# Optimization experiments

Measured on AMD Instinct MI355X. Metric: run time of the kernel, lower is better.

Reference implementation:

```python
import jax, jax.numpy as jnp
import numpy as np
from math import comb

F = 32           # features
NB = 8           # num_basis_functions
N_ITER = 3       # num_iterations
CUTOFF = 5.0
MAXZ = 17        # max_atomic_number
NDCM = 4
N_NODES = 10000
N_EDGES = 160000
OFF = (0, 1, 4)  # start index of degree l block in the (L+1)^2=9 axis
WID = (1, 3, 5)
DEG = np.array([0, 1, 1, 1, 2, 2, 2, 2, 2])


def _sph_harm(u):
    # Real spherical harmonics up to l=2, Racah normalization, cartesian order.
    x, y, z = u[..., 0], u[..., 1], u[..., 2]
    s3 = 3.0 ** 0.5
    return jnp.stack([
        jnp.ones_like(x),
        x, y, z,
        s3 * x * y, s3 * y * z, 0.5 * (3.0 * z * z - 1.0), s3 * x * z,
        0.5 * s3 * (x * x - y * y),
    ], axis=-1)


def _gaunt():
    # Exact Gaunt (triple-product) coupling coefficients via spherical quadrature:
    # Gauss-Legendre (8 pts) in cos(theta) x 16 uniform pts in phi is exact for
    # products of three degree<=2 harmonics. Odd-parity (l1+l2+l3 odd) entries
    # integrate to zero, which matches include_pseudotensors=False.
    t, w = np.polynomial.legendre.leggauss(8)
    phi = np.arange(16) * (2.0 * np.pi / 16.0)
    st = np.sqrt(1.0 - t * t)
    pts = np.stack([
        st[:, None] * np.cos(phi)[None, :],
        st[:, None] * np.sin(phi)[None, :],
        t[:, None] * np.ones_like(phi)[None, :],
    ], axis=-1).reshape(-1, 3)
    wts = np.repeat(w / 32.0, 16)  # mean over sphere
    Y = np.asarray(_sph_harm(jnp.asarray(pts)))
    G = np.einsum('k,kp,kq,kr->pqr', wts, Y, Y, Y)
    G[np.abs(G) < 1e-10] = 0.0
    return G.astype(np.float32)


GAUNT = _gaunt()  # (9, 9, 9)
MP_PATHS = [(a, b, c) for a in range(3) for b in range(3) for c in range(3)
            if (a + b + c) % 2 == 0 and abs(a - b) <= c <= a + b]
TD_PATHS = [p for p in MP_PATHS if p[2] <= 1]


def _blk(l):
    return slice(OFF[l], OFF[l] + WID[l])


def _edge_basis(positions, dst_idx, src_idx):
    d = positions[src_idx] - positions[dst_idx]          # (E, 3)
    r2 = jnp.sum(d * d, axis=-1)
    r = jnp.sqrt(jnp.maximum(r2, 1e-12))
    Y = _sph_harm(d / r[:, None])                        # (E, 9)
    rc = jnp.minimum(r, CUTOFF - 1e-6)                   # safe smooth_cutoff
    cut = jnp.where(r < CUTOFF,
                    jnp.exp(-(rc * rc) / ((CUTOFF - rc) * (CUTOFF + rc))), 0.0)
    yv = 1.0 / (1.0 + r)                                 # reciprocal mapping
    k = jnp.arange(NB)
    binom = jnp.asarray([float(comb(NB - 1, i)) for i in range(NB)], dtype=jnp.float32)
    rbf = binom * yv[:, None] ** k * (1.0 - yv[:, None]) ** (NB - 1 - k)
    return Y, rbf * cut[:, None]                         # (E,9), (E,NB)


def _message_pass(x, Y, rbf, dst_idx, src_idx, W, num_nodes):
    # msg[e,lm3,f] = sum G[lm1,lm2,lm3] x_src[e,lm1,f] Y[e,lm2] (rbf[e] @ W[l1,l2,l3])[f]
    xs = x[src_idx]                                      # (E, 9, F)
    parts = {0: [], 1: [], 2: []}
    for (l1, l2, l3) in MP_PATHS:
        rw = rbf @ W[l1, l2, l3]                         # (E, F) radial weights
        t = xs[:, _blk(l1), :] * rw[:, None, :]
        c = jnp.einsum('pqr,epf,eq->erf',
                       GAUNT[_blk(l1), _blk(l2), _blk(l3)], t, Y[:, _blk(l2)])
        parts[l3].append(c)
    msg = jnp.concatenate([sum(parts[l]) for l in range(3)], axis=1)
    return jax.ops.segment_sum(msg, dst_idx, num_segments=num_nodes)


def _dense(x, W, b):
    out = jnp.einsum('npf,pfg->npg', x, W[DEG])
    return out.at[:, 0, :].add(b)


def _silu_e3(x):
    # Gated equivariant silu: act(s) on scalars, x_lm * act'(s) for l>0.
    s = x[:, 0:1, :]
    sg = jax.nn.sigmoid(s)
    return jnp.concatenate([s * sg, x[:, 1:, :] * (sg * (1.0 + s * (1.0 - sg)))], axis=1)


def _tensor_dense(x, W):
    # with per-path feature-mixing weights; output (N, 4, NDCM).
    parts = {0: [], 1: []}
    for (l1, l2, l3) in TD_PATHS:
        c = jnp.einsum('pqr,npf,nqf,fg->nrg',
                       GAUNT[_blk(l1), _blk(l2), _blk(l3)],
                       x[:, _blk(l1), :], x[:, _blk(l2), :], W[l1, l2, l3])
        parts[l3].append(c)
    return jnp.concatenate([sum(parts[0]), sum(parts[1])], axis=1)


def _forward(positions, embed_table, mp_W, d1_W, d1_b, d2_W, d2_b, td_W,
             mono_W, element_bias, atomic_numbers, dst_idx, src_idx):
    n = positions.shape[0]
    Y, rbf = _edge_basis(positions, dst_idx, src_idx)
    x = jnp.zeros((n, 9, F), positions.dtype).at[:, 0, :].set(embed_table[atomic_numbers])
    for i in range(N_ITER):
        y = x + _message_pass(x, Y, rbf, dst_idx, src_idx, mp_W[i], n)
        y = _silu_e3(_dense(y, d1_W[i], d1_b[i]))
        y = _dense(y, d2_W[i], d2_b[i])
        x = x + y
    x2 = _tensor_dense(x, td_W)                          # (n, 4, NDCM)
    atomic_mono = x2[:, 0, :] @ mono_W + element_bias[atomic_numbers][:, None]
    # gated hard_tanh then * 0.3; dipole = l=1 components
    s = x2[:, 0:1, :]
    gate = ((s > -1.0) & (s < 1.0)).astype(x2.dtype)
    xh = jnp.concatenate([jnp.clip(s, -1.0, 1.0), x2[:, 1:, :] * gate], axis=1) * 0.3
    atomic_dipo = xh[:, 1:4, :]                          # (n, 3, NDCM)
    return atomic_mono, atomic_dipo


def setup_inputs() -> dict:
    key = jax.random.key(0)
    ks = jax.random.split(key, 12)
    atomic_numbers = jax.random.randint(ks[0], (N_NODES,), 0, MAXZ + 1)
    positions = jax.random.normal(ks[1], (N_NODES, 3), jnp.float32)
    dst_idx = jax.random.randint(ks[2], (N_EDGES,), 0, N_NODES)
    src_idx = jax.random.randint(ks[3], (N_EDGES,), 0, N_NODES)
    src_idx = jnp.where(src_idx == dst_idx, (src_idx + 1) % N_NODES, src_idx)
    embed_table = jax.random.normal(ks[4], (MAXZ + 1, F), jnp.float32)
    mp_W = jax.random.normal(ks[5], (N_ITER, 3, 3, 3, NB, F), jnp.float32) * 0.05
    d1_W = jax.random.normal(ks[6], (N_ITER, 3, F, F), jnp.float32) * (1.0 / F ** 0.5)
    d1_b = jnp.zeros((N_ITER, F), jnp.float32)
    d2_W = jax.random.normal(ks[7], (N_ITER, 3, F, F), jnp.float32) * (1.0 / F ** 0.5)
    d2_b = jnp.zeros((N_ITER, F), jnp.float32)
    td_W = jax.random.normal(ks[8], (3, 3, 2, F, NDCM), jnp.float32) * (1.0 / F)
    mono_W = jax.random.normal(ks[9], (NDCM, NDCM), jnp.float32) * (1.0 / NDCM ** 0.5)
    element_bias = jnp.zeros((MAXZ + 1,), jnp.float32)
    return {'positions': positions, 'embed_table': embed_table, 'mp_W': mp_W,
            'd1_W': d1_W, 'd1_b': d1_b, 'd2_W': d2_W, 'd2_b': d2_b,
            'td_W': td_W, 'mono_W': mono_W, 'element_bias': element_bias,
            'atomic_numbers': atomic_numbers, 'dst_idx': dst_idx, 'src_idx': src_idx}


def reference(positions, embed_table, mp_W, d1_W, d1_b, d2_W, d2_b, td_W,
              mono_W, element_bias, atomic_numbers, dst_idx, src_idx):
    return _forward(positions, embed_table, mp_W, d1_W, d1_b, d2_W, d2_b, td_W,
                    mono_W, element_bias, atomic_numbers, dst_idx, src_idx)
```

## Files before the change

### kernel.cpp

```cpp
#include <hip/hip_runtime.h>
#include <math.h>

#define NN 10000
#define NE 160000
#define EPB 8
#define MT 256
#define CEPB 16

namespace {
constexpr int kL1[11] = {0,0,0,1,1,1,1,2,2,2,2};
constexpr int kL2[11] = {0,1,2,0,1,1,2,0,1,2,2};
constexpr int kL3[11] = {0,1,2,1,0,2,1,2,1,0,2};
constexpr int kWOFF[11] = {0,5,7,10,12,14,16,20,22,24,26};
constexpr int tL1[7] = {0,0,1,1,1,2,2};
constexpr int tL2[7] = {0,1,0,1,2,1,2};
constexpr int tL3[7] = {0,1,1,0,1,1,0};
constexpr int kOFF[3] = {0,1,4};
constexpr int kWID[3] = {1,3,5};

struct TVT { unsigned char t[35], p[35]; };
constexpr TVT makeTV() {
  TVT v{};
  int ti = 0;
  for (int t = 0; t < 11; ++t)
    for (int i = 0; i < kWID[kL1[t]]; ++i) {
      v.t[ti] = (unsigned char)t;
      v.p[ti] = (unsigned char)(kOFF[kL1[t]] + i);
      ++ti;
    }
  return v;
}
constexpr TVT TV = makeTV();

struct CTb { unsigned char r[116], tv[116]; };
constexpr CTb makeCT() {
  CTb v{};
  int c = 0, ti = 0;
  for (int t = 0; t < 11; ++t)
    for (int i = 0; i < kWID[kL1[t]]; ++i) {
      for (int k = 0; k < kWID[kL3[t]]; ++k) {
        v.r[c]  = (unsigned char)(kOFF[kL3[t]] + k);
        v.tv[c] = (unsigned char)ti;
        ++c;
      }
      ++ti;
    }
  v.r[115] = 0; v.tv[115] = 0;
  return v;
}
constexpr CTb CTC = makeCT();
}

__device__ float GAUNT_d[729];
__device__ unsigned char CT_P_d[115], CT_R_d[115], CT_L2_d[115];

__device__ __forceinline__ float sphf(int c, float x, float y, float z) {
  const float s3 = 1.7320508075688772f;
  switch (c) {
    case 0: return 1.0f;
    case 1: return x;
    case 2: return y;
    case 3: return z;
    case 4: return s3 * x * y;
    case 5: return s3 * y * z;
    case 6: return 0.5f * (3.0f * z * z - 1.0f);
    case 7: return s3 * x * z;
    default: return 0.5f * s3 * (x * x - y * y);
  }
}

__global__ void gaunt_kernel() {
  __shared__ float Ysh[128][9];
  __shared__ double cph[16], sph[16];
  __shared__ double stq[8], tsh[8], wsh[8];
  const int idx = threadIdx.x;
  const double T[8] = {-0.9602898564975363, -0.7966664774136267, -0.5255324099163290, -0.1834346424956498,
                        0.1834346424956498,  0.5255324099163290,  0.7966664774136267,  0.9602898564975363};
  const double Wq[8] = {0.1012285362903763, 0.2223810344533745, 0.3137066458778873, 0.3626837833783620,
                        0.3626837833783620, 0.3137066458778873, 0.2223810344533745, 0.1012285362903763};
  if (idx < 16) {
    double phi = (double)idx * (6.283185307179586 / 16.0);
    cph[idx] = cos(phi);
    sph[idx] = sin(phi);
  }
  if (idx < 8) {
    tsh[idx] = T[idx];
    wsh[idx] = Wq[idx] / 32.0;
    stq[idx] = sqrt(1.0 - T[idx] * T[idx]);
  }
  __syncthreads();
  for (int i = idx; i < 128 * 9; i += 768) {
    int k = i / 9, c = i - k * 9;
    int it = k >> 4, ip = k & 15;
    float xf = (float)(stq[it] * cph[ip]);
    float yf = (float)(stq[it] * sph[ip]);
    float zf = (float)tsh[it];
    Ysh[k][c] = sphf(c, xf, yf, zf);
  }
  __syncthreads();
  if (idx < 729) {
    int p = idx / 81, q = (idx / 9) % 9, r = idx % 9;
    double acc = 0.0;
    for (int k = 0; k < 128; ++k)
      acc += wsh[k >> 4] * (double)Ysh[k][p] * (double)Ysh[k][q] * (double)Ysh[k][r];
    GAUNT_d[idx] = (fabs(acc) < 1e-10) ? 0.0f : (float)acc;
  }
  if (idx == 0) {
    int c = 0;
    for (int t = 0; t < 11; ++t) {
      int l1 = kL1[t], l2 = kL2[t], l3 = kL3[t];
      for (int i = 0; i < kWID[l1]; ++i)
        for (int k = 0; k < kWID[l3]; ++k) {
          CT_P_d[c]  = (unsigned char)(kOFF[l1] + i);
          CT_R_d[c]  = (unsigned char)(kOFF[l3] + k);
          CT_L2_d[c] = (unsigned char)l2;
          ++c;
        }
    }
  }
}

__global__ void hist_kernel(const int* __restrict__ dstI, int* __restrict__ cnt) {
  int e = blockIdx.x * 256 + threadIdx.x;
  if (e < NE) atomicAdd(&cnt[dstI[e]], 1);
}

__global__ void scan_kernel(int* __restrict__ wofs) {
  __shared__ int partial[1024];
  const int tid = threadIdx.x;
  const int base = tid * 10;
  int local[10];
  int s = 0;
  #pragma unroll
  for (int i = 0; i < 10; ++i) {
    int idx = base + i;
    int v = (idx < NN) ? wofs[idx] : 0;
    local[i] = s;
    s += v;
  }
  partial[tid] = s;
  __syncthreads();
  for (int off = 1; off < 1024; off <<= 1) {
    int v = (tid >= off) ? partial[tid - off] : 0;
    __syncthreads();
    partial[tid] += v;
    __syncthreads();
  }
  int pre = (tid == 0) ? 0 : partial[tid - 1];
  #pragma unroll
  for (int i = 0; i < 10; ++i) {
    int idx = base + i;
    if (idx < NN) wofs[idx] = pre + local[i];
  }
}

__global__ void edge_kernel(const float* __restrict__ pos,
                            const int* __restrict__ srcI, const int* __restrict__ dstI,
                            int* __restrict__ wofs, int* __restrict__ ssrc, int* __restrict__ sdst,
                            float* __restrict__ Yb, float* __restrict__ Rb) {
  int e = blockIdx.x * 256 + threadIdx.x;
  if (e >= NE) return;
  int s = srcI[e], d = dstI[e];
  float dx = pos[s * 3 + 0] - pos[d * 3 + 0];
  float dy = pos[s * 3 + 1] - pos[d * 3 + 1];
  float dz = pos[s * 3 + 2] - pos[d * 3 + 2];
  float r2 = dx * dx + dy * dy + dz * dz;
  float r = sqrtf(fmaxf(r2, 1e-12f));
  float inv = 1.0f / r;
  float x = dx * inv, y = dy * inv, z = dz * inv;
  const float s3 = 1.7320508075688772f;
  int sp = atomicAdd(&wofs[d], 1);
  ssrc[sp] = s;
  sdst[sp] = d;
  Yb[sp * 9 + 0] = 1.0f;
  Yb[sp * 9 + 1] = x;
  Yb[sp * 9 + 2] = y;
  Yb[sp * 9 + 3] = z;
  Yb[sp * 9 + 4] = s3 * x * y;
  Yb[sp * 9 + 5] = s3 * y * z;
  Yb[sp * 9 + 6] = 0.5f * (3.0f * z * z - 1.0f);
  Yb[sp * 9 + 7] = s3 * x * z;
  Yb[sp * 9 + 8] = 0.5f * s3 * (x * x - y * y);
  float rc = fminf(r, 5.0f - 1e-6f);
  float cut = (r < 5.0f) ? expf(-(rc * rc) / ((5.0f - rc) * (5.0f + rc))) : 0.0f;
  float yv = 1.0f / (1.0f + r);
  float om = 1.0f - yv;
  const float binom[8] = {1.f, 7.f, 21.f, 35.f, 35.f, 21.f, 7.f, 1.f};
  float yk[8], ok[8];
  yk[0] = 1.0f; ok[0] = 1.0f;
  #pragma unroll
  for (int k = 1; k < 8; ++k) { yk[k] = yk[k - 1] * yv; ok[k] = ok[k - 1] * om; }
  #pragma unroll
  for (int k = 0; k < 8; ++k) Rb[sp * 8 + k] = binom[k] * yk[k] * ok[7 - k] * cut;
}

__global__ void coef_kernel(const float* __restrict__ Yb, float* __restrict__ Cb) {
  __shared__ float Gs[729];
  __shared__ float Ys[CEPB][9];
  __shared__ unsigned char Tp[115], Tr[115], Tl2[115];
  const int tid = threadIdx.x;
  const int e0 = blockIdx.x * CEPB;
  for (int i = tid; i < 729; i += 256) Gs[i] = GAUNT_d[i];
  for (int i = tid; i < 115; i += 256) { Tp[i] = CT_P_d[i]; Tr[i] = CT_R_d[i]; Tl2[i] = CT_L2_d[i]; }
  for (int i = tid; i < CEPB * 9; i += 256) Ys[i / 9][i % 9] = Yb[e0 * 9 + i];
  __syncthreads();
  for (int i = tid; i < CEPB * 128; i += 256) {
    int ce = i >> 7, c = i & 127;
    if (c < 116) {
      float a = 0.0f;
      if (c < 115) {
        int p = Tp[c], r = Tr[c], l2 = Tl2[c];
        int q0 = (l2 == 0) ? 0 : ((l2 == 1) ? 1 : 4);
        int nq = (l2 == 0) ? 1 : ((l2 == 1) ? 3 : 5);
        for (int j = 0; j < nq; ++j) a += Gs[(p * 9 + q0 + j) * 9 + r] * Ys[ce][q0 + j];
      }
      Cb[(size_t)(e0 + ce) * 116 + c] = a;
    }
  }
}

__global__ void init_kernel(const float* __restrict__ embed, const int* __restrict__ Z,
                            float* __restrict__ xb, float* __restrict__ yb) {
  int idx = blockIdx.x * 256 + threadIdx.x;
  if (idx >= NN * 288) return;
  int n = idx / 288;
  int rem = idx - n * 288;
  int p = rem >> 5, f = rem & 31;
  xb[idx] = (p == 0) ? embed[Z[n] * 32 + f] : 0.0f;
  yb[idx] = 0.0f;
}

__launch_bounds__(MT)
__global__ void message_kernel(const float* __restrict__ xb, float* __restrict__ yb,
                               const float* __restrict__ Rb, const float* __restrict__ Cb,
                               const float* __restrict__ Wg,
                               const int* __restrict__ ssrc, const int* __restrict__ sdst) {
  __shared__ __align__(16) float U[11 * 256];
  __shared__ __align__(16) float4 Cs4[EPB][29];
  __shared__ __align__(16) float Rs[EPB][8];
  __shared__ int Ds[EPB];
  __shared__ int Hs[EPB + 1];
  __shared__ int nseg_s;
  const int tid = threadIdx.x;
  const int e0 = blockIdx.x * EPB;
  const int le = tid >> 5, f = tid & 31;

  const int sn = ssrc[e0 + le];
  float xs[9];
  #pragma unroll
  for (int p = 0; p < 9; ++p) xs[p] = xb[sn * 288 + p * 32 + f];

  float* Ws = U;
  #pragma unroll
  for (int t = 0; t < 11; ++t) {
    const int off = kWOFF[t] * 256;
    Ws[t * 256 + tid] = Wg[off + tid];
  }
  if (tid < EPB * 29) {
    const float4* Cbv = (const float4*)Cb;
    ((float4*)Cs4)[tid] = Cbv[(size_t)e0 * 29 + tid];
  }
  for (int i = tid; i < EPB * 8; i += MT) Rs[i >> 3][i & 7] = Rb[e0 * 8 + i];
  if (tid < EPB) Ds[tid] = sdst[e0 + tid];
  __syncthreads();

  if (tid == 0) {
    int ns = 0;
    #pragma unroll
    for (int i = 0; i < EPB; ++i)
      if (i == 0 || Ds[i] != Ds[i - 1]) Hs[ns++] = i;
    Hs[ns] = EPB;
    nseg_s = ns;
  }

  const float4 R0 = *(const float4*)&Rs[le][0];
  const float4 R1 = *(const float4*)&Rs[le][4];
  float rw[11];
  #pragma unroll
  for (int t = 0; t < 11; ++t) {
    const float* base = &Ws[t * 256];
    rw[t] = R0.x * base[f] + R0.y * base[32 + f] + R0.z * base[64 + f] + R0.w * base[96 + f]
          + R1.x * base[128 + f] + R1.y * base[160 + f] + R1.z * base[192 + f] + R1.w * base[224 + f];
  }

  float tv[35];
  #pragma unroll
  for (int j = 0; j < 35; ++j) tv[j] = rw[TV.t[j]] * xs[TV.p[j]];

  float msg[9] = {0.f, 0.f, 0.f, 0.f, 0.f, 0.f, 0.f, 0.f, 0.f};
  #pragma unroll
  for (int c4 = 0; c4 < 29; ++c4) {
    const float4 cc = Cs4[le][c4];
    const int c = c4 * 4;
    msg[CTC.r[c]] += cc.x * tv[CTC.tv[c]];
    if (c + 1 < 115) msg[CTC.r[c + 1]] += cc.y * tv[CTC.tv[c + 1]];
    if (c + 2 < 115) msg[CTC.r[c + 2]] += cc.z * tv[CTC.tv[c + 2]];
    if (c + 3 < 115) msg[CTC.r[c + 3]] += cc.w * tv[CTC.tv[c + 3]];
  }

  __syncthreads();
  float* Ms = U;
  #pragma unroll
  for (int rr = 0; rr < 9; ++rr) Ms[le * 288 + rr * 32 + f] = msg[rr];
  __syncthreads();

  const int nseg = nseg_s;
  for (int i = tid; i < nseg * 288; i += MT) {
    int s = i / 288, rf = i - s * 288;
    int h = Hs[s], hend = Hs[s + 1];
    float a = 0.0f;
    for (int e = h; e < hend; ++e) a += Ms[e * 288 + rf];
    atomicAdd(&yb[Ds[h] * 288 + rf], a);
  }
}

__launch_bounds__(MT)
__global__ void message_kernel_ic(const float* __restrict__ xb, float* __restrict__ yb,
                                  const float* __restrict__ Yb, const float* __restrict__ Rb,
                                  const float* __restrict__ Wg,
                                  const int* __restrict__ ssrc, const int* __restrict__ sdst) {
  __shared__ float Gs[729];
  __shared__ float Ws[11 * 256];
  __shared__ float Ys[EPB][9];
  __shared__ float Rs[EPB][8];
  __shared__ float Cs[EPB][116];
  __shared__ float Ms[EPB][288];
  __shared__ int Ds[EPB];
  __shared__ int Hs[EPB + 1];
  __shared__ int nseg_s;
  __shared__ unsigned char Tp[115], Tr[115], Tl2[115];
  const int tid = threadIdx.x;
  const int e0 = blockIdx.x * EPB;

  for (int i = tid; i < 729; i += MT) Gs[i] = GAUNT_d[i];
  for (int i = tid; i < 115; i += MT) { Tp[i] = CT_P_d[i]; Tr[i] = CT_R_d[i]; Tl2[i] = CT_L2_d[i]; }
  #pragma unroll
  for (int t = 0; t < 11; ++t) Ws[t * 256 + tid] = Wg[kWOFF[t] * 256 + tid];
  for (int i = tid; i < EPB * 16; i += MT) {
    int le = i >> 4, q = i & 15;
    if (q < 9) Ys[le][q] = Yb[(e0 + le) * 9 + q];
  }
  for (int i = tid; i < EPB * 8; i += MT) Rs[i >> 3][i & 7] = Rb[e0 * 8 + i];
  if (tid < EPB) Ds[tid] = sdst[e0 + tid];
  __syncthreads();

  const int le = tid >> 5, f = tid & 31;
  const int sn = ssrc[e0 + le];
  float xs[9];
  #pragma unroll
  for (int p = 0; p < 9; ++p) xs[p] = xb[sn * 288 + p * 32 + f];

  for (int i = tid; i < EPB * 128; i += MT) {
    int ce = i >> 7, c = i & 127;
    if (c < 115) {
      int p = Tp[c], r = Tr[c], l2 = Tl2[c];
      int q0 = (l2 == 0) ? 0 : ((l2 == 1) ? 1 : 4);
      int nq = (l2 == 0) ? 1 : ((l2 == 1) ? 3 : 5);
      float a = 0.0f;
      for (int j = 0; j < nq; ++j) a += Gs[(p * 9 + q0 + j) * 9 + r] * Ys[ce][q0 + j];
      Cs[ce][c] = a;
    }
  }
  if (tid == 0) {
    int ns = 0;
    #pragma unroll
    for (int i = 0; i < EPB; ++i)
      if (i == 0 || Ds[i] != Ds[i - 1]) Hs[ns++] = i;
    Hs[ns] = EPB;
    nseg_s = ns;
  }
  __syncthreads();

  const float4 R0 = *(const float4*)&Rs[le][0];
  const float4 R1 = *(const float4*)&Rs[le][4];
  float rw[11];
  #pragma unroll
  for (int t = 0; t < 11; ++t) {
    const float* base = &Ws[t * 256];
    rw[t] = R0.x * base[f] + R0.y * base[32 + f] + R0.z * base[64 + f] + R0.w * base[96 + f]
          + R1.x * base[128 + f] + R1.y * base[160 + f] + R1.z * base[192 + f] + R1.w * base[224 + f];
  }
  float tv[35];
  #pragma unroll
  for (int j = 0; j < 35; ++j) tv[j] = rw[TV.t[j]] * xs[TV.p[j]];
  float msg[9] = {0.f, 0.f, 0.f, 0.f, 0.f, 0.f, 0.f, 0.f, 0.f};
  #pragma unroll
  for (int c = 0; c < 115; ++c) msg[CTC.r[c]] += Cs[le][c] * tv[CTC.tv[c]];
  #pragma unroll
  for (int rr = 0; rr < 9; ++rr) Ms[le][rr * 32 + f] = msg[rr];
  __syncthreads();

  const int nseg = nseg_s;
  for (int i = tid; i < nseg * 288; i += MT) {
    int s = i / 288, rf = i - s * 288;
    int h = Hs[s], hend = Hs[s + 1];
    float a = 0.0f;
    for (int e = h; e < hend; ++e) a += Ms[e][rf];
    atomicAdd(&yb[Ds[h] * 288 + rf], a);
  }
}

__global__ void dense_kernel(float* __restrict__ ybuf, float* __restrict__ xb,
                             const float* __restrict__ W1, const float* __restrict__ b1,
                             const float* __restrict__ W2, const float* __restrict__ b2) {
  __shared__ float yn[288];
  __shared__ float act[288];
  __shared__ float sb[32];
  const int n = blockIdx.x;
  const int tid = threadIdx.x;
  const int p = tid >> 5, g = tid & 31;
  const float xv = xb[n * 288 + tid];
  const float yv = ybuf[n * 288 + tid];
  ybuf[n * 288 + tid] = 0.0f;
  yn[tid] = xv + yv;
  __syncthreads();
  const int dg = (p == 0) ? 0 : ((p < 4) ? 1 : 2);
  float a = (p == 0) ? b1[g] : 0.0f;
  #pragma unroll
  for (int f = 0; f < 32; ++f) a += yn[p * 32 + f] * W1[(dg * 32 + f) * 32 + g];
  if (p == 0) sb[g] = a;
  __syncthreads();
  float s = sb[g];
  float sg = 1.0f / (1.0f + expf(-s));
  float v = (p == 0) ? s * sg : a * (sg * (1.0f + s * (1.0f - sg)));
  act[tid] = v;
  __syncthreads();
  float o = (p == 0) ? b2[g] : 0.0f;
  #pragma unroll
  for (int f = 0; f < 32; ++f) o += act[p * 32 + f] * W2[(dg * 32 + f) * 32 + g];
  xb[n * 288 + tid] = xv + o;
}

__global__ void final_kernel(const float* __restrict__ xb, const float* __restrict__ tdW,
                             const float* __restrict__ monoW, const float* __restrict__ ebias,
                             const int* __restrict__ Z, float* __restrict__ out) {
  __shared__ float xl[288];
  __shared__ float B[4][32];
  __shared__ float cb[16];
  const int n = blockIdx.x;
  const int tid = threadIdx.x;
  const int r = tid >> 5, f = tid & 31;
  for (int i = tid; i < 288; i += 128) xl[i] = xb[n * 288 + i];
  __syncthreads();
  float creg = 0.0f;
  #pragma unroll
  for (int t = 0; t < 7; ++t) {
    const int l1 = tL1[t], l2 = tL2[t], l3 = tL3[t];
    const bool active = (l3 == 0) ? (r == 0) : (r >= 1);
    float b = 0.0f;
    if (active) {
      #pragma unroll
      for (int i = 0; i < kWID[l1]; ++i) {
        const int p = kOFF[l1] + i;
        float xp = xl[p * 32 + f];
        #pragma unroll
        for (int j = 0; j < kWID[l2]; ++j) {
          const int q = kOFF[l2] + j;
          b += GAUNT_d[(p * 9 + q) * 9 + r] * xp * xl[q * 32 + f];
        }
      }
    }
    B[r][f] = b;
    __syncthreads();
    if (f < 4 && active) {
      const float* w = tdW + ((l1 * 3 + l2) * 2 + l3) * 128;
      float acc = 0.0f;
      #pragma unroll
      for (int f2 = 0; f2 < 32; ++f2) acc += B[r][f2] * w[f2 * 4 + f];
      creg += acc;
    }
    __syncthreads();
  }
  if (f < 4) cb[r * 4 + f] = creg;
  __syncthreads();
  if (tid < 4) {
    int g = tid;
    float m = 0.0f;
    #pragma unroll
    for (int j = 0; j < 4; ++j) m += cb[j] * monoW[j * 4 + g];
    out[n * 4 + g] = m + ebias[Z[n]];
  }
  if (tid < 12) {
    int row = tid / 4 + 1, g = tid % 4;
    float s = cb[g];
    float gate = (s > -1.0f && s < 1.0f) ? 1.0f : 0.0f;
    out[NN * 4 + n * 12 + (row - 1) * 4 + g] = cb[row * 4 + g] * gate * 0.3f;
  }
}

extern "C" void kernel_launch(void* const* d_in, const int* in_sizes, int n_in,
                              void* d_out, int out_size, void* d_ws, size_t ws_size,
                              hipStream_t stream) {
  const float* positions = (const float*)d_in[0];
  const float* embed     = (const float*)d_in[1];
  const float* mpW       = (const float*)d_in[2];
  const float* d1W       = (const float*)d_in[3];
  const float* d1b       = (const float*)d_in[4];
  const float* d2W       = (const float*)d_in[5];
  const float* d2b       = (const float*)d_in[6];
  const float* tdW       = (const float*)d_in[7];
  const float* monoW     = (const float*)d_in[8];
  const float* ebias     = (const float*)d_in[9];
  const int* Z   = (const int*)d_in[10];
  const int* dst = (const int*)d_in[11];
  const int* src = (const int*)d_in[12];
  float* out = (float*)d_out;

  float* Yb = (float*)d_ws;
  float* Rb = Yb + (size_t)NE * 9;
  float* xb = Rb + (size_t)NE * 8;
  float* yb = xb + (size_t)NN * 288;
  size_t base_f = (size_t)NE * 9 + (size_t)NE * 8 + (size_t)NN * 288 * 2;
  size_t need_pc = (base_f + (size_t)NE * 116) * 4 + ((size_t)NE * 2 + NN) * 4;
  bool pc = ws_size >= need_pc;

  float* Cb = yb + (size_t)NN * 288;
  float* after = pc ? (Cb + (size_t)NE * 116) : Cb;
  int* ssrc = (int*)after;
  int* sdst = ssrc + NE;
  int* wofs = sdst + NE;

  gaunt_kernel<<<1, 768, 0, stream>>>();
  hipMemsetAsync(wofs, 0, NN * sizeof(int), stream);
  hist_kernel<<<NE / 256, 256, 0, stream>>>(dst, wofs);
  scan_kernel<<<1, 1024, 0, stream>>>(wofs);
  edge_kernel<<<NE / 256, 256, 0, stream>>>(positions, src, dst, wofs, ssrc, sdst, Yb, Rb);
  if (pc) coef_kernel<<<NE / CEPB, 256, 0, stream>>>(Yb, Cb);
  init_kernel<<<(NN * 288 + 255) / 256, 256, 0, stream>>>(embed, Z, xb, yb);

  for (int it = 0; it < 3; ++it) {
    if (pc)
      message_kernel<<<NE / EPB, MT, 0, stream>>>(xb, yb, Rb, Cb, mpW + (size_t)it * 27 * 256, ssrc, sdst);
    else
      message_kernel_ic<<<NE / EPB, MT, 0, stream>>>(xb, yb, Yb, Rb, mpW + (size_t)it * 27 * 256, ssrc, sdst);
    dense_kernel<<<NN, 288, 0, stream>>>(yb, xb, d1W + (size_t)it * 3 * 1024, d1b + it * 32,
                                         d2W + (size_t)it * 3 * 1024, d2b + it * 32);
  }
  final_kernel<<<NN, 128, 0, stream>>>(xb, tdW, monoW, ebias, Z, out);
}
```

Before: 431.1 us.

## Process 16 edges per block with two features per thread and fuse final dense

The message kernel now handles 16 edges per 256-thread block, with each thread computing two features as packed float2 vectors. The radial-weight and coupling contraction is restructured to loop directly over path blocks instead of through precomputed tv arrays, and the segmented reduction runs in two halves that reuse the shared buffer. The last iteration's dense update is fused with the final tensor-dipole kernel, removing one launch and a round trip of node features through global memory. Fewer threads per edge and the added half-wise synchronization may reduce parallelism or raise register pressure.

```diff
diff --git a/kernel.cpp b/kernel.cpp
--- a/kernel.cpp
+++ b/kernel.cpp
@@ -3,9 +3,11 @@
 
 #define NN 10000
 #define NE 160000
-#define EPB 8
+#define MEPB 16
 #define MT 256
 #define CEPB 16
+
+typedef float float2v __attribute__((ext_vector_type(2)));
 
 namespace {
 constexpr int kL1[11] = {0,0,0,1,1,1,1,2,2,2,2};
@@ -230,25 +232,26 @@
   yb[idx] = 0.0f;
 }
 
-__launch_bounds__(MT)
+__launch_bounds__(MT, 8)
 __global__ void message_kernel(const float* __restrict__ xb, float* __restrict__ yb,
                                const float* __restrict__ Rb, const float* __restrict__ Cb,
                                const float* __restrict__ Wg,
                                const int* __restrict__ ssrc, const int* __restrict__ sdst) {
   __shared__ __align__(16) float U[11 * 256];
-  __shared__ __align__(16) float4 Cs4[EPB][29];
-  __shared__ __align__(16) float Rs[EPB][8];
-  __shared__ int Ds[EPB];
-  __shared__ int Hs[EPB + 1];
-  __shared__ int nseg_s;
+  __shared__ __align__(16) float Cs[MEPB][116];
+  __shared__ __align__(16) float Rs[MEPB][8];
+  __shared__ int Ds[MEPB];
+  __shared__ int Hs[2][9];
+  __shared__ int nsegS[2];
   const int tid = threadIdx.x;
-  const int e0 = blockIdx.x * EPB;
-  const int le = tid >> 5, f = tid & 31;
+  const int e0 = blockIdx.x * MEPB;
+  const int le = tid >> 4;
+  const int f  = (tid & 15) * 2;
 
   const int sn = ssrc[e0 + le];
-  float xs[9];
-  #pragma unroll
-  for (int p = 0; p < 9; ++p) xs[p] = xb[sn * 288 + p * 32 + f];
+  float2v xs2[9];
+  #pragma unroll
+  for (int p = 0; p < 9; ++p) xs2[p] = *(const float2v*)&xb[sn * 288 + p * 32 + f];
 
   float* Ws = U;
   #pragma unroll
@@ -256,92 +259,106 @@
     const int off = kWOFF[t] * 256;
     Ws[t * 256 + tid] = Wg[off + tid];
   }
-  if (tid < EPB * 29) {
+  {
     const float4* Cbv = (const float4*)Cb;
-    ((float4*)Cs4)[tid] = Cbv[(size_t)e0 * 29 + tid];
-  }
-  for (int i = tid; i < EPB * 8; i += MT) Rs[i >> 3][i & 7] = Rb[e0 * 8 + i];
-  if (tid < EPB) Ds[tid] = sdst[e0 + tid];
+    float4* Csv = (float4*)Cs;
+    #pragma unroll
+    for (int i = tid; i < MEPB * 29; i += MT) Csv[i] = Cbv[(size_t)e0 * 29 + i];
+  }
+  for (int i = tid; i < MEPB * 8; i += MT) Rs[i >> 3][i & 7] = Rb[e0 * 8 + i];
+  if (tid < MEPB) Ds[tid] = sdst[e0 + tid];
   __syncthreads();
 
   if (tid == 0) {
-    int ns = 0;
     #pragma unroll
-    for (int i = 0; i < EPB; ++i)
-      if (i == 0 || Ds[i] != Ds[i - 1]) Hs[ns++] = i;
-    Hs[ns] = EPB;
-    nseg_s = ns;
-  }
-
-  const float4 R0 = *(const float4*)&Rs[le][0];
-  const float4 R1 = *(const float4*)&Rs[le][4];
-  float rw[11];
+    for (int b = 0; b < 2; ++b) {
+      int ns = 0;
+      #pragma unroll
+      for (int i = 0; i < 8; ++i) {
+        int gi = b * 8 + i;
+        if (i == 0 || Ds[gi] != Ds[gi - 1]) Hs[b][ns++] = i;
+      }
+      Hs[b][ns] = 8;
+      nsegS[b] = ns;
+    }
+  }
+
+  float2v msg[9] = {{0.f,0.f},{0.f,0.f},{0.f,0.f},{0.f,0.f},{0.f,0.f},{0.f,0.f},{0.f,0.f},{0.f,0.f},{0.f,0.f}};
+  int c = 0;
   #pragma unroll
   for (int t = 0; t < 11; ++t) {
     const float* base = &Ws[t * 256];
-    rw[t] = R0.x * base[f] + R0.y * base[32 + f] + R0.z * base[64 + f] + R0.w * base[96 + f]
-          + R1.x * base[128 + f] + R1.y * base[160 + f] + R1.z * base[192 + f] + R1.w * base[224 + f];
-  }
-
-  float tv[35];
-  #pragma unroll
-  for (int j = 0; j < 35; ++j) tv[j] = rw[TV.t[j]] * xs[TV.p[j]];
-
-  float msg[9] = {0.f, 0.f, 0.f, 0.f, 0.f, 0.f, 0.f, 0.f, 0.f};
-  #pragma unroll
-  for (int c4 = 0; c4 < 29; ++c4) {
-    const float4 cc = Cs4[le][c4];
-    const int c = c4 * 4;
-    msg[CTC.r[c]] += cc.x * tv[CTC.tv[c]];
-    if (c + 1 < 115) msg[CTC.r[c + 1]] += cc.y * tv[CTC.tv[c + 1]];
-    if (c + 2 < 115) msg[CTC.r[c + 2]] += cc.z * tv[CTC.tv[c + 2]];
-    if (c + 3 < 115) msg[CTC.r[c + 3]] += cc.w * tv[CTC.tv[c + 3]];
-  }
-
-  __syncthreads();
+    float2v acc = {0.f, 0.f};
+    #pragma unroll
+    for (int k = 0; k < 8; ++k) {
+      const float rv = Rs[le][k];
+      const float2v rvv = {rv, rv};
+      const float2v w2 = *(const float2v*)&base[k * 32 + f];
+      acc = acc + rvv * w2;
+    }
+    const int o1 = kOFF[kL1[t]], w1 = kWID[kL1[t]];
+    const int o3 = kOFF[kL3[t]], w3 = kWID[kL3[t]];
+    #pragma unroll
+    for (int i = 0; i < w1; ++i) {
+      const float2v tvv = acc * xs2[o1 + i];
+      #pragma unroll
+      for (int k2 = 0; k2 < w3; ++k2) {
+        const float cc = Cs[le][c]; ++c;
+        const float2v ccv = {cc, cc};
+        msg[o3 + k2] = msg[o3 + k2] + ccv * tvv;
+      }
+    }
+  }
+
   float* Ms = U;
   #pragma unroll
-  for (int rr = 0; rr < 9; ++rr) Ms[le * 288 + rr * 32 + f] = msg[rr];
-  __syncthreads();
-
-  const int nseg = nseg_s;
-  for (int i = tid; i < nseg * 288; i += MT) {
-    int s = i / 288, rf = i - s * 288;
-    int h = Hs[s], hend = Hs[s + 1];
-    float a = 0.0f;
-    for (int e = h; e < hend; ++e) a += Ms[e * 288 + rf];
-    atomicAdd(&yb[Ds[h] * 288 + rf], a);
-  }
-}
-
-__launch_bounds__(MT)
+  for (int b = 0; b < 2; ++b) {
+    __syncthreads();
+    if ((le >> 3) == b) {
+      #pragma unroll
+      for (int rr = 0; rr < 9; ++rr)
+        *(float2v*)&Ms[(le & 7) * 288 + rr * 32 + f] = msg[rr];
+    }
+    __syncthreads();
+    const int ns = nsegS[b];
+    for (int i = tid; i < ns * 288; i += MT) {
+      int s = i / 288, rf = i - s * 288;
+      int h = Hs[b][s], hend = Hs[b][s + 1];
+      float a = 0.0f;
+      for (int e = h; e < hend; ++e) a += Ms[e * 288 + rf];
+      atomicAdd(&yb[Ds[b * 8 + h] * 288 + rf], a);
+    }
+  }
+}
+
+__launch_bounds__(256)
 __global__ void message_kernel_ic(const float* __restrict__ xb, float* __restrict__ yb,
                                   const float* __restrict__ Yb, const float* __restrict__ Rb,
                                   const float* __restrict__ Wg,
                                   const int* __restrict__ ssrc, const int* __restrict__ sdst) {
   __shared__ float Gs[729];
   __shared__ float Ws[11 * 256];
-  __shared__ float Ys[EPB][9];
-  __shared__ float Rs[EPB][8];
-  __shared__ float Cs[EPB][116];
-  __shared__ float Ms[EPB][288];
-  __shared__ int Ds[EPB];
-  __shared__ int Hs[EPB + 1];
+  __shared__ float Ys[8][9];
+  __shared__ float Rs[8][8];
+  __shared__ float Cs[8][116];
+  __shared__ float Ms[8][288];
+  __shared__ int Ds[8];
+  __shared__ int Hs[9];
   __shared__ int nseg_s;
   __shared__ unsigned char Tp[115], Tr[115], Tl2[115];
   const int tid = threadIdx.x;
-  const int e0 = blockIdx.x * EPB;
-
-  for (int i = tid; i < 729; i += MT) Gs[i] = GAUNT_d[i];
-  for (int i = tid; i < 115; i += MT) { Tp[i] = CT_P_d[i]; Tr[i] = CT_R_d[i]; Tl2[i] = CT_L2_d[i]; }
+  const int e0 = blockIdx.x * 8;
+
+  for (int i = tid; i < 729; i += 256) Gs[i] = GAUNT_d[i];
+  for (int i = tid; i < 115; i += 256) { Tp[i] = CT_P_d[i]; Tr[i] = CT_R_d[i]; Tl2[i] = CT_L2_d[i]; }
   #pragma unroll
   for (int t = 0; t < 11; ++t) Ws[t * 256 + tid] = Wg[kWOFF[t] * 256 + tid];
-  for (int i = tid; i < EPB * 16; i += MT) {
+  for (int i = tid; i < 8 * 16; i += 256) {
     int le = i >> 4, q = i & 15;
     if (q < 9) Ys[le][q] = Yb[(e0 + le) * 9 + q];
   }
-  for (int i = tid; i < EPB * 8; i += MT) Rs[i >> 3][i & 7] = Rb[e0 * 8 + i];
-  if (tid < EPB) Ds[tid] = sdst[e0 + tid];
+  for (int i = tid; i < 8 * 8; i += 256) Rs[i >> 3][i & 7] = Rb[e0 * 8 + i];
+  if (tid < 8) Ds[tid] = sdst[e0 + tid];
   __syncthreads();
 
   const int le = tid >> 5, f = tid & 31;
@@ -350,7 +367,7 @@
   #pragma unroll
   for (int p = 0; p < 9; ++p) xs[p] = xb[sn * 288 + p * 32 + f];
 
-  for (int i = tid; i < EPB * 128; i += MT) {
+  for (int i = tid; i < 8 * 128; i += 256) {
     int ce = i >> 7, c = i & 127;
     if (c < 115) {
       int p = Tp[c], r = Tr[c], l2 = Tl2[c];
@@ -364,9 +381,9 @@
   if (tid == 0) {
     int ns = 0;
     #pragma unroll
-    for (int i = 0; i < EPB; ++i)
+    for (int i = 0; i < 8; ++i)
       if (i == 0 || Ds[i] != Ds[i - 1]) Hs[ns++] = i;
-    Hs[ns] = EPB;
+    Hs[ns] = 8;
     nseg_s = ns;
   }
   __syncthreads();
@@ -391,7 +408,7 @@
   __syncthreads();
 
   const int nseg = nseg_s;
-  for (int i = tid; i < nseg * 288; i += MT) {
+  for (int i = tid; i < nseg * 288; i += 256) {
     int s = i / 288, rf = i - s * 288;
     int h = Hs[s], hend = Hs[s + 1];
     float a = 0.0f;
@@ -431,60 +448,86 @@
   xb[n * 288 + tid] = xv + o;
 }
 
-__global__ void final_kernel(const float* __restrict__ xb, const float* __restrict__ tdW,
-                             const float* __restrict__ monoW, const float* __restrict__ ebias,
-                             const int* __restrict__ Z, float* __restrict__ out) {
-  __shared__ float xl[288];
+__global__ void dense_final_kernel(const float* __restrict__ ybuf, const float* __restrict__ xb,
+                                   const float* __restrict__ W1, const float* __restrict__ b1,
+                                   const float* __restrict__ W2, const float* __restrict__ b2,
+                                   const float* __restrict__ tdW, const float* __restrict__ monoW,
+                                   const float* __restrict__ ebias, const int* __restrict__ Z,
+                                   float* __restrict__ out) {
+  __shared__ float yn[288];
+  __shared__ float act[288];
+  __shared__ float sb[32];
   __shared__ float B[4][32];
   __shared__ float cb[16];
   const int n = blockIdx.x;
   const int tid = threadIdx.x;
-  const int r = tid >> 5, f = tid & 31;
-  for (int i = tid; i < 288; i += 128) xl[i] = xb[n * 288 + i];
-  __syncthreads();
+  const int p = tid >> 5, g = tid & 31;
+  const float xv = xb[n * 288 + tid];
+  const float yv = ybuf[n * 288 + tid];
+  yn[tid] = xv + yv;
+  __syncthreads();
+  const int dg = (p == 0) ? 0 : ((p < 4) ? 1 : 2);
+  float a = (p == 0) ? b1[g] : 0.0f;
+  #pragma unroll
+  for (int f = 0; f < 32; ++f) a += yn[p * 32 + f] * W1[(dg * 32 + f) * 32 + g];
+  if (p == 0) sb[g] = a;
+  __syncthreads();
+  float s = sb[g];
+  float sg = 1.0f / (1.0f + expf(-s));
+  float v = (p == 0) ? s * sg : a * (sg * (1.0f + s * (1.0f - sg)));
+  act[tid] = v;
+  __syncthreads();
+  float o = (p == 0) ? b2[g] : 0.0f;
+  #pragma unroll
+  for (int f = 0; f < 32; ++f) o += act[p * 32 + f] * W2[(dg * 32 + f) * 32 + g];
+  const float xnew = xv + o;
+  __syncthreads();
+  yn[tid] = xnew;
+  __syncthreads();
+
   float creg = 0.0f;
   #pragma unroll
   for (int t = 0; t < 7; ++t) {
     const int l1 = tL1[t], l2 = tL2[t], l3 = tL3[t];
-    const bool active = (l3 == 0) ? (r == 0) : (r >= 1);
+    const bool active = (tid < 128) && ((l3 == 0) ? (p == 0) : (p >= 1));
     float b = 0.0f;
     if (active) {
       #pragma unroll
       for (int i = 0; i < kWID[l1]; ++i) {
-        const int p = kOFF[l1] + i;
-        float xp = xl[p * 32 + f];
+        const int pp = kOFF[l1] + i;
+        float xp = yn[pp * 32 + g];
         #pragma unroll
         for (int j = 0; j < kWID[l2]; ++j) {
           const int q = kOFF[l2] + j;
-          b += GAUNT_d[(p * 9 + q) * 9 + r] * xp * xl[q * 32 + f];
+          b += GAUNT_d[(pp * 9 + q) * 9 + p] * xp * yn[q * 32 + g];
         }
       }
     }
-    B[r][f] = b;
+    if (tid < 128) B[p][g] = b;
     __syncthreads();
-    if (f < 4 && active) {
+    if (active && g < 4) {
       const float* w = tdW + ((l1 * 3 + l2) * 2 + l3) * 128;
       float acc = 0.0f;
       #pragma unroll
-      for (int f2 = 0; f2 < 32; ++f2) acc += B[r][f2] * w[f2 * 4 + f];
+      for (int f2 = 0; f2 < 32; ++f2) acc += B[p][f2] * w[f2 * 4 + g];
       creg += acc;
     }
     __syncthreads();
   }
-  if (f < 4) cb[r * 4 + f] = creg;
+  if (tid < 128 && g < 4) cb[p * 4 + g] = creg;
   __syncthreads();
   if (tid < 4) {
-    int g = tid;
+    int gg = tid;
     float m = 0.0f;
     #pragma unroll
-    for (int j = 0; j < 4; ++j) m += cb[j] * monoW[j * 4 + g];
-    out[n * 4 + g] = m + ebias[Z[n]];
+    for (int j = 0; j < 4; ++j) m += cb[j] * monoW[j * 4 + gg];
+    out[n * 4 + gg] = m + ebias[Z[n]];
   }
   if (tid < 12) {
-    int row = tid / 4 + 1, g = tid % 4;
-    float s = cb[g];
-    float gate = (s > -1.0f && s < 1.0f) ? 1.0f : 0.0f;
-    out[NN * 4 + n * 12 + (row - 1) * 4 + g] = cb[row * 4 + g] * gate * 0.3f;
+    int row = tid / 4 + 1, gg = tid % 4;
+    float sv = cb[gg];
+    float gate = (sv > -1.0f && sv < 1.0f) ? 1.0f : 0.0f;
+    out[NN * 4 + n * 12 + (row - 1) * 4 + gg] = cb[row * 4 + gg] * gate * 0.3f;
   }
 }
 
@@ -530,11 +573,15 @@
 
   for (int it = 0; it < 3; ++it) {
     if (pc)
-      message_kernel<<<NE / EPB, MT, 0, stream>>>(xb, yb, Rb, Cb, mpW + (size_t)it * 27 * 256, ssrc, sdst);
+      message_kernel<<<NE / MEPB, MT, 0, stream>>>(xb, yb, Rb, Cb, mpW + (size_t)it * 27 * 256, ssrc, sdst);
     else
-      message_kernel_ic<<<NE / EPB, MT, 0, stream>>>(xb, yb, Yb, Rb, mpW + (size_t)it * 27 * 256, ssrc, sdst);
-    dense_kernel<<<NN, 288, 0, stream>>>(yb, xb, d1W + (size_t)it * 3 * 1024, d1b + it * 32,
-                                         d2W + (size_t)it * 3 * 1024, d2b + it * 32);
-  }
-  final_kernel<<<NN, 128, 0, stream>>>(xb, tdW, monoW, ebias, Z, out);
-}
+      message_kernel_ic<<<NE / 8, 256, 0, stream>>>(xb, yb, Yb, Rb, mpW + (size_t)it * 27 * 256, ssrc, sdst);
+    if (it < 2)
+      dense_kernel<<<NN, 288, 0, stream>>>(yb, xb, d1W + (size_t)it * 3 * 1024, d1b + it * 32,
+                                           d2W + (size_t)it * 3 * 1024, d2b + it * 32);
+    else
+      dense_final_kernel<<<NN, 288, 0, stream>>>(yb, xb, d1W + (size_t)it * 3 * 1024, d1b + it * 32,
+                                                 d2W + (size_t)it * 3 * 1024, d2b + it * 32,
+                                                 tdW, monoW, ebias, Z, out);
+  }
+}
```

Measured after the change: 433.8 us. Within noise of the previous version (+0.6%).
